# Kernel optimization log

Hardware: AMD Instinct MI355X
Metric: run time of the kernel (lower is better)

Reference implementation:

```python
import jax, jax.numpy as jnp
import numpy as np

D_MODEL = 1024
BATCH = 4
SEQ = 4096

def setup_inputs() -> dict:
    key = jax.random.key(0)
    k1, k2, k3, k4 = jax.random.split(key, 4)
    scale = 1.0 / np.sqrt(D_MODEL)
    return {
        "inp_emb": jax.random.normal(k1, (BATCH, SEQ, D_MODEL), dtype=jnp.float32),
        "Wq": jax.random.normal(k2, (D_MODEL, D_MODEL), dtype=jnp.float32) * scale,
        "Wk": jax.random.normal(k3, (D_MODEL, D_MODEL), dtype=jnp.float32) * scale,
        "Wv": jax.random.normal(k4, (D_MODEL, D_MODEL), dtype=jnp.float32) * scale,
    }

def reference(inp_emb, Wq, Wk, Wv):
    d_model = Wq.shape[0]
    # torch Linear (no bias): y = x @ W.T
    Q = jnp.einsum('bsd,ed->bse', inp_emb, Wq)
    K = jnp.einsum('bsd,ed->bse', inp_emb, Wk)
    V = jnp.einsum('bsd,ed->bse', inp_emb, Wv)
    scores = jnp.einsum('bqd,bkd->bqk', Q, K) / jnp.sqrt(jnp.float32(d_model))
    probs = jax.nn.softmax(scores, axis=2)
    return jnp.einsum('bqk,bkd->bqd', probs, V)
```

## Files before the change

### kernel.cpp

```cpp
#include <hip/hip_runtime.h>


typedef __bf16 bf16_t;
typedef __bf16 bf16x8 __attribute__((ext_vector_type(8)));
typedef float f32x4 __attribute__((ext_vector_type(4)));

typedef __attribute__((address_space(3))) void lds_void_t;
typedef __attribute__((address_space(1))) void gbl_void_t;

#define SEQ 4096
#define DM  1024

__global__ __launch_bounds__(256) void cast_f32_to_bf16(
    const float* __restrict__ in, bf16_t* __restrict__ out, int n8)
{
    int idx = blockIdx.x * 256 + threadIdx.x;
    if (idx >= n8) return;
    long i = (long)idx * 8;
    f32x4 a = *(const f32x4*)(in + i);
    f32x4 b = *(const f32x4*)(in + i + 4);
    bf16x8 o;
    o[0] = (bf16_t)a[0]; o[1] = (bf16_t)a[1]; o[2] = (bf16_t)a[2]; o[3] = (bf16_t)a[3];
    o[4] = (bf16_t)b[0]; o[5] = (bf16_t)b[1]; o[6] = (bf16_t)b[2]; o[7] = (bf16_t)b[3];
    *(bf16x8*)(out + i) = o;
}

__global__ __launch_bounds__(256) void cast3_w(
    const float* __restrict__ w0, const float* __restrict__ w1,
    const float* __restrict__ w2, bf16_t* __restrict__ out)
{
    const float* in = (blockIdx.z == 0) ? w0 : (blockIdx.z == 1) ? w1 : w2;
    long i = ((long)blockIdx.x * 256 + threadIdx.x) * 8;
    f32x4 a = *(const f32x4*)(in + i);
    f32x4 b = *(const f32x4*)(in + i + 4);
    bf16x8 o;
    o[0] = (bf16_t)a[0]; o[1] = (bf16_t)a[1]; o[2] = (bf16_t)a[2]; o[3] = (bf16_t)a[3];
    o[4] = (bf16_t)b[0]; o[5] = (bf16_t)b[1]; o[6] = (bf16_t)b[2]; o[7] = (bf16_t)b[3];
    *(bf16x8*)(out + (long)blockIdx.z * 1048576 + i) = o;
}

__global__ __launch_bounds__(256) void zero_f32(float* __restrict__ p, int n)
{
    int idx = blockIdx.x * 256 + threadIdx.x;
    if (idx < n) p[idx] = 0.f;
}

template <typename TOUT, int MODE>
__global__ __launch_bounds__(256, 4) void gemm_bt(
    const bf16_t* __restrict__ A, int lda, long sAz,
    const bf16_t* __restrict__ B, int ldb, long sBz,
    TOUT* __restrict__ C, int ldc, long sCz,
    int K, float scale, float* __restrict__ l, long sLz)
{
    __shared__ bf16_t As[128 * 32];
    __shared__ bf16_t Bs[128 * 32];

    A += (long)blockIdx.z * sAz;
    B += (long)blockIdx.z * sBz;
    C += (long)blockIdx.z * sCz;

    const int tid  = threadIdx.x;
    const int wave = tid >> 6;
    const int lane = tid & 63;
    const int m0 = blockIdx.x * 128;
    const int n0 = blockIdx.y * 128;
    const int wm = (wave >> 1) * 64;
    const int wn = (wave & 1) * 64;
    const int mrow = lane & 15;
    const int koff = (lane >> 4) * 8;

    f32x4 acc[4][4];
#pragma unroll
    for (int i = 0; i < 4; ++i)
#pragma unroll
        for (int j = 0; j < 4; ++j)
            acc[i][j] = (f32x4){0.f, 0.f, 0.f, 0.f};

    const int c0 = wave * 2;

    for (int k0 = 0; k0 < K; k0 += 32) {
#pragma unroll
        for (int t = 0; t < 2; ++t) {
            const int chunk = c0 + t;
            const int flat  = chunk * 64 + lane;
            const int row   = flat >> 2;
            const int kp    = (flat & 3) * 8;
            const bf16_t* ga = A + (long)(m0 + row) * lda + (k0 + kp);
            const bf16_t* gb = B + (long)(n0 + row) * ldb + (k0 + kp);
            __builtin_amdgcn_global_load_lds((const gbl_void_t*)ga,
                                             (lds_void_t*)(As + chunk * 512), 16, 0, 0);
            __builtin_amdgcn_global_load_lds((const gbl_void_t*)gb,
                                             (lds_void_t*)(Bs + chunk * 512), 16, 0, 0);
        }
        __syncthreads();

        bf16x8 af[4], bfr[4];
#pragma unroll
        for (int i = 0; i < 4; ++i)
            af[i] = *(const bf16x8*)(As + (wm + i * 16 + mrow) * 32 + koff);
#pragma unroll
        for (int j = 0; j < 4; ++j)
            bfr[j] = *(const bf16x8*)(Bs + (wn + j * 16 + mrow) * 32 + koff);
#pragma unroll
        for (int i = 0; i < 4; ++i)
#pragma unroll
            for (int j = 0; j < 4; ++j)
                acc[i][j] = __builtin_amdgcn_mfma_f32_16x16x32_bf16(af[i], bfr[j], acc[i][j], 0, 0, 0);
        __syncthreads();
    }

    const int col = lane & 15;
    const int r0  = (lane >> 4) * 4;

    if (MODE == 1) {
#pragma unroll
        for (int i = 0; i < 4; ++i)
#pragma unroll
            for (int r = 0; r < 4; ++r) {
                float s = 0.f;
#pragma unroll
                for (int j = 0; j < 4; ++j) {
                    float e = __expf(acc[i][j][r] * scale);
                    acc[i][j][r] = e;
                    s += e;
                }
                s += __shfl_xor(s, 1);
                s += __shfl_xor(s, 2);
                s += __shfl_xor(s, 4);
                s += __shfl_xor(s, 8);
                if (col == 0)
                    atomicAdd(&l[(long)blockIdx.z * sLz + m0 + wm + i * 16 + r0 + r], s);
            }
#pragma unroll
        for (int i = 0; i < 4; ++i)
#pragma unroll
            for (int j = 0; j < 4; ++j)
#pragma unroll
                for (int r = 0; r < 4; ++r)
                    C[(long)(m0 + wm + i * 16 + r0 + r) * ldc + (n0 + wn + j * 16 + col)] =
                        (TOUT)acc[i][j][r];
    } else if (MODE == 2) {
        float inv[4][4];
#pragma unroll
        for (int i = 0; i < 4; ++i)
#pragma unroll
            for (int r = 0; r < 4; ++r)
                inv[i][r] = scale / l[(long)blockIdx.z * sLz + m0 + wm + i * 16 + r0 + r];
#pragma unroll
        for (int i = 0; i < 4; ++i)
#pragma unroll
            for (int j = 0; j < 4; ++j)
#pragma unroll
                for (int r = 0; r < 4; ++r)
                    C[(long)(m0 + wm + i * 16 + r0 + r) * ldc + (n0 + wn + j * 16 + col)] =
                        (TOUT)(acc[i][j][r] * inv[i][r]);
    } else {
#pragma unroll
        for (int i = 0; i < 4; ++i)
#pragma unroll
            for (int j = 0; j < 4; ++j)
#pragma unroll
                for (int r = 0; r < 4; ++r)
                    C[(long)(m0 + wm + i * 16 + r0 + r) * ldc + (n0 + wn + j * 16 + col)] =
                        (TOUT)(acc[i][j][r] * scale);
    }
}

template <typename TOUT, int MODE>
__global__ __launch_bounds__(512, 2) void gemm_big256(
    const bf16_t* __restrict__ A, int lda, long sAz,
    const bf16_t* __restrict__ B, int ldb, long sBz,
    TOUT* __restrict__ C, int ldc, long sCz,
    int K, float scale, float* __restrict__ l, long sLz)
{
    __shared__ __align__(1024) char smem[98304];

    A += (long)blockIdx.z * sAz;
    B += (long)blockIdx.z * sBz;
    C += (long)blockIdx.z * sCz;

    const int tid  = threadIdx.x;
    const int wave = tid >> 6;
    const int lane = tid & 63;
    const int m0 = blockIdx.x * 256;
    const int n0 = blockIdx.y * 256;
    const int wm = (wave >> 2) * 128;
    const int wn = (wave & 3) * 64;

    const int srow = wave * 16 + (lane >> 2);
    const int skk  = ((lane & 3) * 8) ^ ((lane & 32) ? 16 : 0);
    const bf16_t* gA0 = A + (long)(m0 + srow) * lda + skk;
    const bf16_t* gA1 = A + (long)(m0 + srow + 128) * lda + skk;
    const bf16_t* gB0 = B + (long)(n0 + srow) * ldb + skk;
    const bf16_t* gB1 = B + (long)(n0 + srow + 128) * ldb + skk;
    char* ldsA = smem + wave * 1024;
    char* ldsB = smem + 49152 + wave * 1024;

    auto stage_A = [&](int kt, int d) {
        const int k0 = kt << 5;
        __builtin_amdgcn_global_load_lds((const gbl_void_t*)(gA0 + k0),
                                         (lds_void_t*)(ldsA + d * 16384), 16, 0, 0);
        __builtin_amdgcn_global_load_lds((const gbl_void_t*)(gA1 + k0),
                                         (lds_void_t*)(ldsA + d * 16384 + 8192), 16, 0, 0);
    };
    auto stage_B = [&](int kt, int d) {
        const int k0 = kt << 5;
        __builtin_amdgcn_global_load_lds((const gbl_void_t*)(gB0 + k0),
                                         (lds_void_t*)(ldsB + d * 16384), 16, 0, 0);
        __builtin_amdgcn_global_load_lds((const gbl_void_t*)(gB1 + k0),
                                         (lds_void_t*)(ldsB + d * 16384 + 8192), 16, 0, 0);
    };

    const int kswz = ((lane >> 4) * 16) ^ ((lane & 8) ? 32 : 0);
    const int aoff = (wm + (lane & 15)) * 64 + kswz;
    const int boff = (wn + (lane & 15)) * 64 + kswz;

    f32x4 acc[8][4];
#pragma unroll
    for (int i = 0; i < 8; ++i)
#pragma unroll
        for (int j = 0; j < 4; ++j)
            acc[i][j] = (f32x4){0.f, 0.f, 0.f, 0.f};

    const int NT = K >> 5;

    stage_A(0, 0); stage_B(0, 0);
    if (NT > 1) {
        stage_A(1, 1); stage_B(1, 1);
        asm volatile("s_waitcnt vmcnt(4)" ::: "memory");
    } else {
        asm volatile("s_waitcnt vmcnt(0)" ::: "memory");
    }
    __builtin_amdgcn_s_barrier();

    int cur = 0, nxt = 2;
    for (int t = 0; t < NT; ++t) {
        const char* pa = smem + cur * 16384 + aoff;
        const char* pb = smem + 49152 + cur * 16384 + boff;

        bf16x8 bfr[4], af[4];
#pragma unroll
        for (int j = 0; j < 4; ++j) bfr[j] = *(const bf16x8*)(pb + j * 1024);
#pragma unroll
        for (int i = 0; i < 4; ++i) af[i] = *(const bf16x8*)(pa + i * 1024);
        if (t + 2 < NT) stage_A(t + 2, nxt);
        __builtin_amdgcn_s_setprio(1);
#pragma unroll
        for (int i = 0; i < 4; ++i)
#pragma unroll
            for (int j = 0; j < 4; ++j)
                acc[i][j] = __builtin_amdgcn_mfma_f32_16x16x32_bf16(af[i], bfr[j], acc[i][j], 0, 0, 0);
        __builtin_amdgcn_s_setprio(0);

        bf16x8 af2[4];
#pragma unroll
        for (int i = 0; i < 4; ++i) af2[i] = *(const bf16x8*)(pa + 4096 + i * 1024);
        if (t + 2 < NT) stage_B(t + 2, nxt);
        __builtin_amdgcn_s_setprio(1);
#pragma unroll
        for (int i = 0; i < 4; ++i)
#pragma unroll
            for (int j = 0; j < 4; ++j)
                acc[4 + i][j] = __builtin_amdgcn_mfma_f32_16x16x32_bf16(af2[i], bfr[j], acc[4 + i][j], 0, 0, 0);
        __builtin_amdgcn_s_setprio(0);

        __builtin_amdgcn_sched_barrier(0);
        if (t + 2 < NT)
            asm volatile("s_waitcnt vmcnt(4) lgkmcnt(0)" ::: "memory");
        else if (t + 1 < NT)
            asm volatile("s_waitcnt vmcnt(0) lgkmcnt(0)" ::: "memory");
        else
            asm volatile("s_waitcnt lgkmcnt(0)" ::: "memory");
        __builtin_amdgcn_s_barrier();
        cur = (cur == 2) ? 0 : cur + 1;
        nxt = (nxt == 2) ? 0 : nxt + 1;
    }

    const int col = lane & 15;
    const int r0  = (lane >> 4) * 4;

    if (MODE == 1) {
#pragma unroll
        for (int i = 0; i < 8; ++i)
#pragma unroll
            for (int r = 0; r < 4; ++r) {
                float s = 0.f;
#pragma unroll
                for (int j = 0; j < 4; ++j) {
                    float e = __expf(acc[i][j][r] * scale);
                    acc[i][j][r] = e;
                    s += e;
                }
                s += __shfl_xor(s, 1);
                s += __shfl_xor(s, 2);
                s += __shfl_xor(s, 4);
                s += __shfl_xor(s, 8);
                if (col == 0)
                    atomicAdd(&l[(long)blockIdx.z * sLz + m0 + wm + i * 16 + r0 + r], s);
            }
#pragma unroll
        for (int i = 0; i < 8; ++i)
#pragma unroll
            for (int j = 0; j < 4; ++j)
#pragma unroll
                for (int r = 0; r < 4; ++r)
                    C[(long)(m0 + wm + i * 16 + r0 + r) * ldc + (n0 + wn + j * 16 + col)] =
                        (TOUT)acc[i][j][r];
    } else if (MODE == 2) {
        float inv[8][4];
#pragma unroll
        for (int i = 0; i < 8; ++i)
#pragma unroll
            for (int r = 0; r < 4; ++r)
                inv[i][r] = scale / l[(long)blockIdx.z * sLz + m0 + wm + i * 16 + r0 + r];
#pragma unroll
        for (int i = 0; i < 8; ++i)
#pragma unroll
            for (int j = 0; j < 4; ++j)
#pragma unroll
                for (int r = 0; r < 4; ++r)
                    C[(long)(m0 + wm + i * 16 + r0 + r) * ldc + (n0 + wn + j * 16 + col)] =
                        (TOUT)(acc[i][j][r] * inv[i][r]);
    } else {
#pragma unroll
        for (int i = 0; i < 8; ++i)
#pragma unroll
            for (int j = 0; j < 4; ++j)
#pragma unroll
                for (int r = 0; r < 4; ++r)
                    C[(long)(m0 + wm + i * 16 + r0 + r) * ldc + (n0 + wn + j * 16 + col)] =
                        (TOUT)(acc[i][j][r] * scale);
    }
}

template <typename TOUT, int MODE, int LDA, int LDB, int LDC>
__global__ __launch_bounds__(512, 4) void gemm_bt256(
    const bf16_t* __restrict__ A, long sAz,
    const bf16_t* __restrict__ B, long sBz,
    TOUT* __restrict__ C, long sCz,
    int K, float scale, float* __restrict__ l, long sLz)
{
    __shared__ __align__(1024) char smem[73728];

    A += (long)blockIdx.z * sAz;
    B += (long)blockIdx.z * sBz;
    C += (long)blockIdx.z * sCz;

    const int m0 = blockIdx.x * 256;
    const int n0 = blockIdx.y * 128;

    const int tid  = threadIdx.x;
    const int wave = tid >> 6;
    const int lane = tid & 63;
    const int wm = (wave >> 2) * 128;
    const int wn = (wave & 3) * 32;

    const int srow = wave * 16 + (lane >> 2);
    const int ksrc = (((lane & 3) ^ ((lane >> 3) & 3)) << 3);
    const bf16_t* pa0 = A + (long)(m0 + srow) * LDA + ksrc;
    const bf16_t* pa1 = pa0 + (long)128 * LDA;
    const bf16_t* pb0 = B + (long)(n0 + srow) * LDB + ksrc;
    const int ldsw = wave * 1024;

    const int kterm = (((lane >> 4) ^ ((lane >> 1) & 3)) << 4);
    const int aoff = (wm + (lane & 15)) * 64 + kterm;
    const int boff = (wn + (lane & 15)) * 64 + kterm;

    f32x4 acc[8][2];
#pragma unroll
    for (int i = 0; i < 8; ++i)
#pragma unroll
        for (int j = 0; j < 2; ++j)
            acc[i][j] = (f32x4){0.f, 0.f, 0.f, 0.f};

    const int NT = K >> 5;

#define STAGE_A2(buf)                                                          \
    do {                                                                       \
        __builtin_amdgcn_global_load_lds((const gbl_void_t*)pa0,               \
            (lds_void_t*)(smem + (buf)*16384 + ldsw), 16, 0, 0);               \
        __builtin_amdgcn_global_load_lds((const gbl_void_t*)pa1,               \
            (lds_void_t*)(smem + (buf)*16384 + 8192 + ldsw), 16, 0, 0);        \
    } while (0)
#define STAGE_B1(buf)                                                          \
    __builtin_amdgcn_global_load_lds((const gbl_void_t*)pb0,                   \
        (lds_void_t*)(smem + 49152 + (buf)*8192 + ldsw), 16, 0, 0)

    STAGE_A2(0); STAGE_B1(0); pa0 += 32; pa1 += 32; pb0 += 32;
    if (NT > 1) {
        STAGE_A2(1); STAGE_B1(1); pa0 += 32; pa1 += 32; pb0 += 32;
        asm volatile("s_waitcnt vmcnt(3)" ::: "memory");
    } else {
        asm volatile("s_waitcnt vmcnt(0)" ::: "memory");
    }
    __builtin_amdgcn_sched_barrier(0);
    __builtin_amdgcn_s_barrier();

    int cur = 0, sb = 2;
    for (int t = 0; t < NT; ++t) {
        const char* Ab = smem + cur * 16384;
        const char* Bb = smem + 49152 + cur * 8192;
        const bool more = (t + 2 < NT);

        bf16x8 bfr[2], af[4];
#pragma unroll
        for (int j = 0; j < 2; ++j) bfr[j] = *(const bf16x8*)(Bb + boff + j * 1024);
#pragma unroll
        for (int i = 0; i < 4; ++i) af[i] = *(const bf16x8*)(Ab + aoff + i * 1024);
        if (more) STAGE_A2(sb);
        asm volatile("s_waitcnt lgkmcnt(0)" ::: "memory");
        __builtin_amdgcn_sched_barrier(0);
        __builtin_amdgcn_s_setprio(1);
#pragma unroll
        for (int i = 0; i < 4; ++i)
#pragma unroll
            for (int j = 0; j < 2; ++j)
                acc[i][j] = __builtin_amdgcn_mfma_f32_16x16x32_bf16(af[i], bfr[j], acc[i][j], 0, 0, 0);
        __builtin_amdgcn_s_setprio(0);

#pragma unroll
        for (int i = 0; i < 4; ++i) af[i] = *(const bf16x8*)(Ab + aoff + 4096 + i * 1024);
        if (more) STAGE_B1(sb);
        asm volatile("s_waitcnt lgkmcnt(0)" ::: "memory");
        __builtin_amdgcn_sched_barrier(0);
        __builtin_amdgcn_s_setprio(1);
#pragma unroll
        for (int i = 0; i < 4; ++i)
#pragma unroll
            for (int j = 0; j < 2; ++j)
                acc[4 + i][j] = __builtin_amdgcn_mfma_f32_16x16x32_bf16(af[i], bfr[j], acc[4 + i][j], 0, 0, 0);
        __builtin_amdgcn_s_setprio(0);

        if (more) {
            asm volatile("s_waitcnt vmcnt(3)" ::: "memory");
            pa0 += 32; pa1 += 32; pb0 += 32;
        } else if (t + 1 < NT) {
            asm volatile("s_waitcnt vmcnt(0)" ::: "memory");
        }
        __builtin_amdgcn_sched_barrier(0);
        __builtin_amdgcn_s_barrier();
        cur = (cur == 2) ? 0 : cur + 1;
        sb  = (sb == 2) ? 0 : sb + 1;
    }
#undef STAGE_A2
#undef STAGE_B1

    const int col = lane & 15;
    const int r0  = (lane >> 4) * 4;

    if (MODE == 1) {
#pragma unroll
        for (int i = 0; i < 8; ++i)
#pragma unroll
            for (int r = 0; r < 4; ++r) {
                float s = 0.f;
#pragma unroll
                for (int j = 0; j < 2; ++j) {
                    float e = __expf(acc[i][j][r] * scale);
                    acc[i][j][r] = e;
                    s += e;
                }
                s += __shfl_xor(s, 1);
                s += __shfl_xor(s, 2);
                s += __shfl_xor(s, 4);
                s += __shfl_xor(s, 8);
                if (col == 0)
                    atomicAdd(&l[(long)blockIdx.z * sLz + m0 + wm + i * 16 + r0 + r], s);
            }
#pragma unroll
        for (int i = 0; i < 8; ++i)
#pragma unroll
            for (int j = 0; j < 2; ++j)
#pragma unroll
                for (int r = 0; r < 4; ++r)
                    C[(long)(m0 + wm + i * 16 + r0 + r) * LDC + (n0 + wn + j * 16 + col)] =
                        (TOUT)acc[i][j][r];
    } else if (MODE == 2) {
        float inv[8][4];
#pragma unroll
        for (int i = 0; i < 8; ++i)
#pragma unroll
            for (int r = 0; r < 4; ++r)
                inv[i][r] = scale / l[(long)blockIdx.z * sLz + m0 + wm + i * 16 + r0 + r];
#pragma unroll
        for (int i = 0; i < 8; ++i)
#pragma unroll
            for (int j = 0; j < 2; ++j)
#pragma unroll
                for (int r = 0; r < 4; ++r)
                    C[(long)(m0 + wm + i * 16 + r0 + r) * LDC + (n0 + wn + j * 16 + col)] =
                        (TOUT)(acc[i][j][r] * inv[i][r]);
    } else {
#pragma unroll
        for (int i = 0; i < 8; ++i)
#pragma unroll
            for (int j = 0; j < 2; ++j)
#pragma unroll
                for (int r = 0; r < 4; ++r)
                    C[(long)(m0 + wm + i * 16 + r0 + r) * LDC + (n0 + wn + j * 16 + col)] =
                        (TOUT)(acc[i][j][r] * scale);
    }
}

__device__ __forceinline__ float waveMax(float v)
{
#pragma unroll
    for (int o = 32; o > 0; o >>= 1) v = fmaxf(v, __shfl_xor(v, o));
    return v;
}
__device__ __forceinline__ float waveSum(float v)
{
#pragma unroll
    for (int o = 32; o > 0; o >>= 1) v += __shfl_xor(v, o);
    return v;
}

__global__ __launch_bounds__(256) void softmax_rows(bf16_t* __restrict__ S)
{
    const long row = blockIdx.x;
    bf16_t* p = S + row * SEQ;
    const int tid = threadIdx.x;

    float v[16];
    bf16x8 a0 = *(const bf16x8*)(p + tid * 16);
    bf16x8 a1 = *(const bf16x8*)(p + tid * 16 + 8);
#pragma unroll
    for (int i = 0; i < 8; ++i) { v[i] = (float)a0[i]; v[8 + i] = (float)a1[i]; }

    float m = -1e30f;
#pragma unroll
    for (int i = 0; i < 16; ++i) m = fmaxf(m, v[i]);

    __shared__ float redm[4];
    __shared__ float reds[4];
    m = waveMax(m);
    if ((tid & 63) == 0) redm[tid >> 6] = m;
    __syncthreads();
    m = fmaxf(fmaxf(redm[0], redm[1]), fmaxf(redm[2], redm[3]));

    float s = 0.f;
#pragma unroll
    for (int i = 0; i < 16; ++i) { v[i] = __expf(v[i] - m); s += v[i]; }
    s = waveSum(s);
    if ((tid & 63) == 0) reds[tid >> 6] = s;
    __syncthreads();
    s = reds[0] + reds[1] + reds[2] + reds[3];
    const float inv = 1.0f / s;

    bf16x8 o0, o1;
#pragma unroll
    for (int i = 0; i < 8; ++i) {
        o0[i] = (bf16_t)(v[i] * inv);
        o1[i] = (bf16_t)(v[8 + i] * inv);
    }
    *(bf16x8*)(p + tid * 16)     = o0;
    *(bf16x8*)(p + tid * 16 + 8) = o1;
}

__global__ __launch_bounds__(256) void transpose_bf16(
    const bf16_t* __restrict__ in, int ldin, long sInZ,
    bf16_t* __restrict__ out, int ldout, long sOutZ)
{
    in  += (long)blockIdx.z * sInZ;
    out += (long)blockIdx.z * sOutZ;
    __shared__ bf16_t t[32][33];
    const int tx = threadIdx.x;
    const int ty = threadIdx.y;
    const int x  = blockIdx.x * 32 + tx;
    const int y0 = blockIdx.y * 32;
#pragma unroll
    for (int i = 0; i < 4; ++i)
        t[ty + i * 8][tx] = in[(long)(y0 + ty + i * 8) * ldin + x];
    __syncthreads();
    const int xo = blockIdx.x * 32;
#pragma unroll
    for (int i = 0; i < 4; ++i)
        out[(long)(xo + ty + i * 8) * ldout + y0 + tx] = t[tx][ty + i * 8];
}

extern "C" void kernel_launch(void* const* d_in, const int* in_sizes, int n_in,
                              void* d_out, int out_size, void* d_ws, size_t ws_size,
                              hipStream_t stream)
{
    const float* X  = (const float*)d_in[0];
    const float* Wq = (const float*)d_in[1];
    const float* Wk = (const float*)d_in[2];
    const float* Wv = (const float*)d_in[3];
    float* out = (float*)d_out;
    char* ws = (char*)d_ws;

    if (ws_size >= (256ull << 20)) {
        bf16_t* Xbf  = (bf16_t*)ws;
        bf16_t* Vbf  = (bf16_t*)(ws + (32l << 20));
        bf16_t* Tbuf = (bf16_t*)(ws + (32l << 20));
        bf16_t* VT   = (bf16_t*)(ws + (64l << 20));
        bf16_t* Sbuf = (bf16_t*)(ws + (96l << 20));
        bf16_t* Wall = (bf16_t*)(ws + (224l << 20));
        bf16_t* WqT  = (bf16_t*)(ws + (230l << 20));
        bf16_t* WkT  = (bf16_t*)(ws + (232l << 20));
        bf16_t* Mt   = (bf16_t*)(ws + (234l << 20));
        float*  lbuf = (float*)(ws + (236l << 20));

        cast_f32_to_bf16<<<(16777216 / 8) / 256, 256, 0, stream>>>(X, Xbf, 16777216 / 8);
        cast3_w<<<dim3(512, 1, 3), 256, 0, stream>>>(Wq, Wk, Wv, Wall);

        transpose_bf16<<<dim3(32, 32, 2), dim3(32, 8), 0, stream>>>(
            Wall, DM, 1048576, WqT, DM, 1048576);

        gemm_bt<bf16_t, 0><<<dim3(8, 8, 1), 256, 0, stream>>>(
            WkT, DM, 0l, WqT, DM, 0l, Mt, DM, 0l, DM, 1.0f, nullptr, 0l);

        gemm_big256<bf16_t, 0><<<dim3(64, 4, 1), 512, 0, stream>>>(
            Xbf, DM, 0l, Wall + 2097152, DM, 0l, Vbf, DM, 0l, DM, 1.0f, nullptr, 0l);

        transpose_bf16<<<dim3(DM / 32, SEQ / 32, 4), dim3(32, 8), 0, stream>>>(
            Vbf, DM, (long)SEQ * DM, VT, SEQ, (long)DM * SEQ);

        gemm_big256<bf16_t, 0><<<dim3(64, 4, 1), 512, 0, stream>>>(
            Xbf, DM, 0l, Mt, DM, 0l, Tbuf, DM, 0l, DM, 1.0f, nullptr, 0l);

        zero_f32<<<64, 256, 0, stream>>>(lbuf, 4 * SEQ);

        gemm_bt256<bf16_t, 1, DM, DM, SEQ><<<dim3(16, 32, 4), 512, 0, stream>>>(
            Tbuf, (long)SEQ * DM,
            Xbf, (long)SEQ * DM,
            Sbuf, (long)SEQ * SEQ, DM, 0.03125f, lbuf, SEQ);

        gemm_big256<float, 2><<<dim3(16, 4, 4), 512, 0, stream>>>(
            Sbuf, SEQ, (long)SEQ * SEQ,
            VT, SEQ, (long)DM * SEQ,
            out, DM, (long)SEQ * DM, SEQ, 1.0f, lbuf, SEQ);
    } else {
        bf16_t* Sbuf = (bf16_t*)ws;
        bf16_t* Xbf  = (bf16_t*)ws;
        bf16_t* Wall = (bf16_t*)(ws + (33l << 20));
        bf16_t* QKV  = (bf16_t*)(ws + (40l << 20));
        bf16_t* VT   = (bf16_t*)(ws + (137l << 20));

        cast_f32_to_bf16<<<(16777216 / 8) / 256, 256, 0, stream>>>(X, Xbf, 16777216 / 8);
        cast3_w<<<dim3(512, 1, 3), 256, 0, stream>>>(Wq, Wk, Wv, Wall);

        gemm_bt<bf16_t, 0><<<dim3(128, 24, 1), 256, 0, stream>>>(
            Xbf, DM, 0l, Wall, DM, 0l, QKV, 3072, 0l, DM, 1.0f, nullptr, 0l);

        for (int b = 0; b < 4; ++b) {
            const bf16_t* Qb = QKV + (long)b * SEQ * 3072;
            gemm_bt<bf16_t, 0><<<dim3(32, 32, 1), 256, 0, stream>>>(
                Qb, 3072, 0l, Qb + 1024, 3072, 0l, Sbuf, SEQ, 0l, DM, 0.03125f, nullptr, 0l);
            softmax_rows<<<SEQ, 256, 0, stream>>>(Sbuf);
            transpose_bf16<<<dim3(DM / 32, SEQ / 32, 1), dim3(32, 8), 0, stream>>>(
                Qb + 2048, 3072, 0l, VT, SEQ, 0l);
            gemm_bt<float, 0><<<dim3(32, 8, 1), 256, 0, stream>>>(
                Sbuf, SEQ, 0l, VT, SEQ, 0l, out + (long)b * SEQ * DM, DM, 0l, SEQ, 1.0f, nullptr, 0l);
        }
    }
}
```

Measured before the change: 510.3 us.

## Replace 256x256 GEMM with 128x256 tile kernel for higher occupancy

Replaces the 256x256-tile gemm_big256 with gemm_mn, which uses 128x256 tiles, less LDS, compile-time leading dimensions, a new XOR swizzle and a restructured load/MFMA interleave. It targets better occupancy (launch bounds 4 instead of 2) and more blocks for the V/T projections and the final PV GEMM, where the old grid had only 256 blocks. In exchange each tile reuses B less, so global/L2 traffic per FLOP rises, and the extra lgkmcnt waits may expose LDS latency.

```diff
diff --git a/kernel.cpp b/kernel.cpp
--- a/kernel.cpp
+++ b/kernel.cpp
@@ -166,122 +166,124 @@
     }
 }
 
-template <typename TOUT, int MODE>
-__global__ __launch_bounds__(512, 2) void gemm_big256(
-    const bf16_t* __restrict__ A, int lda, long sAz,
-    const bf16_t* __restrict__ B, int ldb, long sBz,
-    TOUT* __restrict__ C, int ldc, long sCz,
+template <typename TOUT, int MODE, int LDA, int LDB, int LDC>
+__global__ __launch_bounds__(512, 4) void gemm_mn(
+    const bf16_t* __restrict__ A, long sAz,
+    const bf16_t* __restrict__ B, long sBz,
+    TOUT* __restrict__ C, long sCz,
     int K, float scale, float* __restrict__ l, long sLz)
 {
-    __shared__ __align__(1024) char smem[98304];
+    __shared__ __align__(1024) char smem[73728];
 
     A += (long)blockIdx.z * sAz;
     B += (long)blockIdx.z * sBz;
     C += (long)blockIdx.z * sCz;
 
+    const int m0 = blockIdx.x * 128;
+    const int n0 = blockIdx.y * 256;
+
     const int tid  = threadIdx.x;
     const int wave = tid >> 6;
     const int lane = tid & 63;
-    const int m0 = blockIdx.x * 256;
-    const int n0 = blockIdx.y * 256;
-    const int wm = (wave >> 2) * 128;
+    const int wm = (wave >> 2) * 64;
     const int wn = (wave & 3) * 64;
 
     const int srow = wave * 16 + (lane >> 2);
-    const int skk  = ((lane & 3) * 8) ^ ((lane & 32) ? 16 : 0);
-    const bf16_t* gA0 = A + (long)(m0 + srow) * lda + skk;
-    const bf16_t* gA1 = A + (long)(m0 + srow + 128) * lda + skk;
-    const bf16_t* gB0 = B + (long)(n0 + srow) * ldb + skk;
-    const bf16_t* gB1 = B + (long)(n0 + srow + 128) * ldb + skk;
-    char* ldsA = smem + wave * 1024;
-    char* ldsB = smem + 49152 + wave * 1024;
-
-    auto stage_A = [&](int kt, int d) {
-        const int k0 = kt << 5;
-        __builtin_amdgcn_global_load_lds((const gbl_void_t*)(gA0 + k0),
-                                         (lds_void_t*)(ldsA + d * 16384), 16, 0, 0);
-        __builtin_amdgcn_global_load_lds((const gbl_void_t*)(gA1 + k0),
-                                         (lds_void_t*)(ldsA + d * 16384 + 8192), 16, 0, 0);
-    };
-    auto stage_B = [&](int kt, int d) {
-        const int k0 = kt << 5;
-        __builtin_amdgcn_global_load_lds((const gbl_void_t*)(gB0 + k0),
-                                         (lds_void_t*)(ldsB + d * 16384), 16, 0, 0);
-        __builtin_amdgcn_global_load_lds((const gbl_void_t*)(gB1 + k0),
-                                         (lds_void_t*)(ldsB + d * 16384 + 8192), 16, 0, 0);
-    };
-
-    const int kswz = ((lane >> 4) * 16) ^ ((lane & 8) ? 32 : 0);
-    const int aoff = (wm + (lane & 15)) * 64 + kswz;
-    const int boff = (wn + (lane & 15)) * 64 + kswz;
-
-    f32x4 acc[8][4];
-#pragma unroll
-    for (int i = 0; i < 8; ++i)
+    const int ksrc = (((lane & 3) ^ ((lane >> 3) & 3)) << 3);
+    const bf16_t* pa0 = A + (long)(m0 + srow) * LDA + ksrc;
+    const bf16_t* pb0 = B + (long)(n0 + srow) * LDB + ksrc;
+    const bf16_t* pb1 = pb0 + (long)128 * LDB;
+    const int ldsw = wave * 1024;
+
+    const int kterm = (((lane >> 4) ^ ((lane >> 1) & 3)) << 4);
+    const int aoff = (wm + (lane & 15)) * 64 + kterm;
+    const int boff = (wn + (lane & 15)) * 64 + kterm;
+
+    f32x4 acc[4][4];
+#pragma unroll
+    for (int i = 0; i < 4; ++i)
 #pragma unroll
         for (int j = 0; j < 4; ++j)
             acc[i][j] = (f32x4){0.f, 0.f, 0.f, 0.f};
 
     const int NT = K >> 5;
 
-    stage_A(0, 0); stage_B(0, 0);
+#define STAGE_A1(buf)                                                          \
+    __builtin_amdgcn_global_load_lds((const gbl_void_t*)pa0,                   \
+        (lds_void_t*)(smem + (buf)*8192 + ldsw), 16, 0, 0)
+#define STAGE_B2(buf)                                                          \
+    do {                                                                       \
+        __builtin_amdgcn_global_load_lds((const gbl_void_t*)pb0,               \
+            (lds_void_t*)(smem + 24576 + (buf)*16384 + ldsw), 16, 0, 0);       \
+        __builtin_amdgcn_global_load_lds((const gbl_void_t*)pb1,               \
+            (lds_void_t*)(smem + 24576 + (buf)*16384 + 8192 + ldsw), 16, 0, 0);\
+    } while (0)
+
+    STAGE_A1(0); STAGE_B2(0); pa0 += 32; pb0 += 32; pb1 += 32;
     if (NT > 1) {
-        stage_A(1, 1); stage_B(1, 1);
-        asm volatile("s_waitcnt vmcnt(4)" ::: "memory");
+        STAGE_A1(1); STAGE_B2(1); pa0 += 32; pb0 += 32; pb1 += 32;
+        asm volatile("s_waitcnt vmcnt(3)" ::: "memory");
     } else {
         asm volatile("s_waitcnt vmcnt(0)" ::: "memory");
     }
+    __builtin_amdgcn_sched_barrier(0);
     __builtin_amdgcn_s_barrier();
 
-    int cur = 0, nxt = 2;
+    int cur = 0, sb = 2;
     for (int t = 0; t < NT; ++t) {
-        const char* pa = smem + cur * 16384 + aoff;
-        const char* pb = smem + 49152 + cur * 16384 + boff;
-
-        bf16x8 bfr[4], af[4];
-#pragma unroll
-        for (int j = 0; j < 4; ++j) bfr[j] = *(const bf16x8*)(pb + j * 1024);
-#pragma unroll
-        for (int i = 0; i < 4; ++i) af[i] = *(const bf16x8*)(pa + i * 1024);
-        if (t + 2 < NT) stage_A(t + 2, nxt);
+        const char* Ab = smem + cur * 8192;
+        const char* Bb = smem + 24576 + cur * 16384;
+        const bool more = (t + 2 < NT);
+
+        bf16x8 af[4], bfr[2];
+#pragma unroll
+        for (int i = 0; i < 4; ++i) af[i] = *(const bf16x8*)(Ab + aoff + i * 1024);
+#pragma unroll
+        for (int j = 0; j < 2; ++j) bfr[j] = *(const bf16x8*)(Bb + boff + j * 1024);
+        if (more) STAGE_B2(sb);
+        asm volatile("s_waitcnt lgkmcnt(0)" ::: "memory");
+        __builtin_amdgcn_sched_barrier(0);
         __builtin_amdgcn_s_setprio(1);
 #pragma unroll
         for (int i = 0; i < 4; ++i)
 #pragma unroll
-            for (int j = 0; j < 4; ++j)
+            for (int j = 0; j < 2; ++j)
                 acc[i][j] = __builtin_amdgcn_mfma_f32_16x16x32_bf16(af[i], bfr[j], acc[i][j], 0, 0, 0);
         __builtin_amdgcn_s_setprio(0);
 
-        bf16x8 af2[4];
-#pragma unroll
-        for (int i = 0; i < 4; ++i) af2[i] = *(const bf16x8*)(pa + 4096 + i * 1024);
-        if (t + 2 < NT) stage_B(t + 2, nxt);
+#pragma unroll
+        for (int j = 0; j < 2; ++j) bfr[j] = *(const bf16x8*)(Bb + boff + 2048 + j * 1024);
+        if (more) STAGE_A1(sb);
+        asm volatile("s_waitcnt lgkmcnt(0)" ::: "memory");
+        __builtin_amdgcn_sched_barrier(0);
         __builtin_amdgcn_s_setprio(1);
 #pragma unroll
         for (int i = 0; i < 4; ++i)
 #pragma unroll
-            for (int j = 0; j < 4; ++j)
-                acc[4 + i][j] = __builtin_amdgcn_mfma_f32_16x16x32_bf16(af2[i], bfr[j], acc[4 + i][j], 0, 0, 0);
+            for (int j = 0; j < 2; ++j)
+                acc[i][2 + j] = __builtin_amdgcn_mfma_f32_16x16x32_bf16(af[i], bfr[j], acc[i][2 + j], 0, 0, 0);
         __builtin_amdgcn_s_setprio(0);
 
+        if (more) {
+            asm volatile("s_waitcnt vmcnt(3)" ::: "memory");
+            pa0 += 32; pb0 += 32; pb1 += 32;
+        } else if (t + 1 < NT) {
+            asm volatile("s_waitcnt vmcnt(0)" ::: "memory");
+        }
         __builtin_amdgcn_sched_barrier(0);
-        if (t + 2 < NT)
-            asm volatile("s_waitcnt vmcnt(4) lgkmcnt(0)" ::: "memory");
-        else if (t + 1 < NT)
-            asm volatile("s_waitcnt vmcnt(0) lgkmcnt(0)" ::: "memory");
-        else
-            asm volatile("s_waitcnt lgkmcnt(0)" ::: "memory");
         __builtin_amdgcn_s_barrier();
         cur = (cur == 2) ? 0 : cur + 1;
-        nxt = (nxt == 2) ? 0 : nxt + 1;
-    }
+        sb  = (sb == 2) ? 0 : sb + 1;
+    }
+#undef STAGE_A1
+#undef STAGE_B2
 
     const int col = lane & 15;
     const int r0  = (lane >> 4) * 4;
 
     if (MODE == 1) {
 #pragma unroll
-        for (int i = 0; i < 8; ++i)
+        for (int i = 0; i < 4; ++i)
 #pragma unroll
             for (int r = 0; r < 4; ++r) {
                 float s = 0.f;
@@ -299,36 +301,36 @@
                     atomicAdd(&l[(long)blockIdx.z * sLz + m0 + wm + i * 16 + r0 + r], s);
             }
 #pragma unroll
-        for (int i = 0; i < 8; ++i)
+        for (int i = 0; i < 4; ++i)
 #pragma unroll
             for (int j = 0; j < 4; ++j)
 #pragma unroll
                 for (int r = 0; r < 4; ++r)
-                    C[(long)(m0 + wm + i * 16 + r0 + r) * ldc + (n0 + wn + j * 16 + col)] =
+                    C[(long)(m0 + wm + i * 16 + r0 + r) * LDC + (n0 + wn + j * 16 + col)] =
                         (TOUT)acc[i][j][r];
     } else if (MODE == 2) {
-        float inv[8][4];
-#pragma unroll
-        for (int i = 0; i < 8; ++i)
+        float inv[4][4];
+#pragma unroll
+        for (int i = 0; i < 4; ++i)
 #pragma unroll
             for (int r = 0; r < 4; ++r)
                 inv[i][r] = scale / l[(long)blockIdx.z * sLz + m0 + wm + i * 16 + r0 + r];
 #pragma unroll
-        for (int i = 0; i < 8; ++i)
+        for (int i = 0; i < 4; ++i)
 #pragma unroll
             for (int j = 0; j < 4; ++j)
 #pragma unroll
                 for (int r = 0; r < 4; ++r)
-                    C[(long)(m0 + wm + i * 16 + r0 + r) * ldc + (n0 + wn + j * 16 + col)] =
+                    C[(long)(m0 + wm + i * 16 + r0 + r) * LDC + (n0 + wn + j * 16 + col)] =
                         (TOUT)(acc[i][j][r] * inv[i][r]);
     } else {
 #pragma unroll
-        for (int i = 0; i < 8; ++i)
+        for (int i = 0; i < 4; ++i)
 #pragma unroll
             for (int j = 0; j < 4; ++j)
 #pragma unroll
                 for (int r = 0; r < 4; ++r)
-                    C[(long)(m0 + wm + i * 16 + r0 + r) * ldc + (n0 + wn + j * 16 + col)] =
+                    C[(long)(m0 + wm + i * 16 + r0 + r) * LDC + (n0 + wn + j * 16 + col)] =
                         (TOUT)(acc[i][j][r] * scale);
     }
 }
@@ -610,14 +612,14 @@
         gemm_bt<bf16_t, 0><<<dim3(8, 8, 1), 256, 0, stream>>>(
             WkT, DM, 0l, WqT, DM, 0l, Mt, DM, 0l, DM, 1.0f, nullptr, 0l);
 
-        gemm_big256<bf16_t, 0><<<dim3(64, 4, 1), 512, 0, stream>>>(
-            Xbf, DM, 0l, Wall + 2097152, DM, 0l, Vbf, DM, 0l, DM, 1.0f, nullptr, 0l);
+        gemm_mn<bf16_t, 0, DM, DM, DM><<<dim3(128, 4, 1), 512, 0, stream>>>(
+            Xbf, 0l, Wall + 2097152, 0l, Vbf, 0l, DM, 1.0f, nullptr, 0l);
 
         transpose_bf16<<<dim3(DM / 32, SEQ / 32, 4), dim3(32, 8), 0, stream>>>(
             Vbf, DM, (long)SEQ * DM, VT, SEQ, (long)DM * SEQ);
 
-        gemm_big256<bf16_t, 0><<<dim3(64, 4, 1), 512, 0, stream>>>(
-            Xbf, DM, 0l, Mt, DM, 0l, Tbuf, DM, 0l, DM, 1.0f, nullptr, 0l);
+        gemm_mn<bf16_t, 0, DM, DM, DM><<<dim3(128, 4, 1), 512, 0, stream>>>(
+            Xbf, 0l, Mt, 0l, Tbuf, 0l, DM, 1.0f, nullptr, 0l);
 
         zero_f32<<<64, 256, 0, stream>>>(lbuf, 4 * SEQ);
 
@@ -626,10 +628,10 @@
             Xbf, (long)SEQ * DM,
             Sbuf, (long)SEQ * SEQ, DM, 0.03125f, lbuf, SEQ);
 
-        gemm_big256<float, 2><<<dim3(16, 4, 4), 512, 0, stream>>>(
-            Sbuf, SEQ, (long)SEQ * SEQ,
-            VT, SEQ, (long)DM * SEQ,
-            out, DM, (long)SEQ * DM, SEQ, 1.0f, lbuf, SEQ);
+        gemm_mn<float, 2, SEQ, SEQ, DM><<<dim3(32, 4, 4), 512, 0, stream>>>(
+            Sbuf, (long)SEQ * SEQ,
+            VT, (long)DM * SEQ,
+            out, (long)SEQ * DM, SEQ, 1.0f, lbuf, SEQ);
     } else {
         bf16_t* Sbuf = (bf16_t*)ws;
         bf16_t* Xbf  = (bf16_t*)ws;
```

After: 530.5 us. +4.0%, slower.
